# Kernel optimization log

Hardware: AMD Instinct MI355X
Metric: run time of the kernel (lower is better)

The kernel has to match this reference:

```python
import jax, jax.numpy as jnp
import numpy as np

NUM_LEVELS = 4
RADIUS = 4


def _sample1d(vol, x):
    """Linear interpolation along width with zeros padding (grid_sample bilinear,
    align_corners=True, on a height-1 image reduces to this).
    vol: [N, W], x: [N, S] absolute x-coordinates. Returns [N, S]."""
    W = vol.shape[1]
    x0 = jnp.floor(x)
    t = x - x0
    i0 = x0.astype(jnp.int32)
    i1 = i0 + 1

    def gather(i):
        v = jnp.take_along_axis(vol, jnp.clip(i, 0, W - 1), axis=1)
        return jnp.where((i >= 0) & (i < W), v, jnp.zeros_like(v))

    return gather(i0) * (1.0 - t) + gather(i1) * t


def setup_inputs() -> dict:
    key = jax.random.key(0)
    k1, k2, k3 = jax.random.split(key, 3)
    B, C, h, w = 4, 256, 96, 320
    fmap1 = jax.random.normal(k1, (B, C, h, w), dtype=jnp.float32)
    fmap2 = jax.random.normal(k2, (B, C, h, w), dtype=jnp.float32)
    # absolute x-coordinates of centroids, in [0, w-1]
    centroids_coords = jax.random.uniform(k3, (B, 1, h, w), dtype=jnp.float32) * (w - 1)
    return {"fmap1": fmap1, "fmap2": fmap2, "centroids_coords": centroids_coords}


def reference(fmap1, fmap2, centroids_coords):
    B, C, h, w = fmap1.shape
    # 1D correlation volume: dot product over channels, per row, all width pairs
    corr = jnp.einsum('bchw,bchv->bhwv', fmap1, fmap2)  # [B, h, w, w]
    corr = corr / jnp.sqrt(jnp.asarray(C, fmap1.dtype))
    vol = corr.reshape(B * h * w, w)  # [N, w], one 1D row-correlation per query pixel

    cent = centroids_coords.transpose(0, 2, 3, 1).reshape(B * h * w)  # [N]
    side = 2 * RADIUS + 1
    di = jnp.linspace(-RADIUS, RADIUS, side).astype(fmap1.dtype)  # [side]

    outs = []
    for lvl in range(NUM_LEVELS):
        x = cent[:, None] + di[None, :]  # [N, side] absolute coords at this level
        outs.append(_sample1d(vol, x).reshape(B, h, w, side))
        if lvl < NUM_LEVELS - 1:
            Wl = vol.shape[1]
            # avg_pool2d kernel (1,2) stride (1,2) along width
            vol = vol[:, : (Wl // 2) * 2].reshape(vol.shape[0], Wl // 2, 2).mean(axis=2)
            cent = cent / 2.0

    corr_features = jnp.concatenate(outs, axis=-1).transpose(0, 3, 1, 2)
    return corr_features  # [B, num_levels*(2r+1), h, w]
```

## Files before the change

### kernel.cpp

```cpp
#include <hip/hip_runtime.h>

#define W_ 320
#define H_ 96
#define B_ 4
#define C_ 256
#define CS (H_ * W_)
#define MT_ 160
#define PITCH 34
#define PITCHC 321
#define ABUF (MT_ * PITCH)
#define BBUF (W_ * PITCH)
#define TBUF (ABUF + BBUF)

typedef __attribute__((ext_vector_type(8))) short short8;
typedef __attribute__((ext_vector_type(4))) float f32x4;

static __device__ __forceinline__ unsigned f2bf(float f) {
  unsigned u = __builtin_bit_cast(unsigned, f);
  return (u + 0x7FFFu + ((u >> 16) & 1u)) >> 16;
}
static __device__ __forceinline__ unsigned pk(float a, float b) {
  return f2bf(a) | (f2bf(b) << 16);
}
static __device__ __forceinline__ float bf2f(unsigned short h) {
  return __builtin_bit_cast(float, (unsigned)h << 16);
}

union Frag { short8 s; uint4 u; };

__global__ __launch_bounds__(512, 2) void corr_row(
    const float* __restrict__ fmap1, const float* __restrict__ fmap2,
    const float* __restrict__ cents, float* __restrict__ out)
{
  __shared__ __align__(16) unsigned short smem[2 * TBUF];
  unsigned short* Csh = smem;

  const int tid  = threadIdx.x;
  const int lane = tid & 63;
  const int wv   = tid >> 6;
  const int mw   = wv >> 2;
  const int nw   = wv & 3;
  const int m    = lane & 15;
  const int quad = lane >> 4;

  const int i    = blockIdx.x;
  const int r    = ((i >> 4) << 3) | (i & 7);
  const int half = (i >> 3) & 1;
  const int b    = r / H_;
  const int hh   = r % H_;
  const int q0   = half * MT_;

  const float* Abase = fmap1 + ((size_t)b * C_ * H_ + hh) * W_ + q0;
  const float* Bbase = fmap2 + ((size_t)b * C_ * H_ + hh) * W_;

  const float* sp[4];
  int dsti[4];
  int dstsel[4];
  bool act[4];
#pragma unroll
  for (int p = 0; p < 4; ++p) {
    int it = tid + 512 * p;
    act[p] = (it < 1920);
    int c2, v0;
    bool isA = (it < 640);
    if (isA) { c2 = it / 40; v0 = (it % 40) * 4; }
    else     { int ib = it - 640; c2 = ib / 80; v0 = (ib % 80) * 4; }
    if (!act[p]) { c2 = 0; v0 = 0; }
    sp[p]     = (isA ? Abase : Bbase) + (size_t)(2 * c2) * CS + v0;
    dsti[p]   = v0 * 17 + c2;
    dstsel[p] = isA ? 0 : (ABUF / 2);
  }

  f32x4 acc[5][5] = {};
  Frag fa[5];

  float4 g0[4][2], g1[4][2];

  auto issue = [&](int s, float4 (*g)[2]) {
#pragma unroll
    for (int p = 0; p < 4; ++p)
      if (act[p]) {
        const float* q = sp[p] + (size_t)(s * 32) * CS;
        g[p][0] = *(const float4*)q;
        g[p][1] = *(const float4*)(q + CS);
      }
  };
  auto stage = [&](int s, float4 (*g)[2]) {
    unsigned* buf = (unsigned*)(smem + (s & 1) * TBUF);
#pragma unroll
    for (int p = 0; p < 4; ++p)
      if (act[p]) {
        unsigned* d = buf + dstsel[p] + dsti[p];
        d[0]      = pk(g[p][0].x, g[p][1].x);
        d[17]     = pk(g[p][0].y, g[p][1].y);
        d[2 * 17] = pk(g[p][0].z, g[p][1].z);
        d[3 * 17] = pk(g[p][0].w, g[p][1].w);
      }
  };
  auto fragmfma = [&](int s) {
    const unsigned* buf = (const unsigned*)(smem + (s & 1) * TBUF);
#pragma unroll
    for (int mt = 0; mt < 5; ++mt) {
      const unsigned* pa = buf + (mw * 80 + mt * 16 + m) * 17 + quad * 4;
      fa[mt].u.x = pa[0]; fa[mt].u.y = pa[1]; fa[mt].u.z = pa[2]; fa[mt].u.w = pa[3];
    }
#pragma unroll
    for (int nt = 0; nt < 5; ++nt) {
      const unsigned* pb = buf + (ABUF / 2) + (nw * 80 + nt * 16 + m) * 17 + quad * 4;
      Frag fb;
      fb.u.x = pb[0]; fb.u.y = pb[1]; fb.u.z = pb[2]; fb.u.w = pb[3];
#pragma unroll
      for (int mt = 0; mt < 5; ++mt)
        acc[mt][nt] = __builtin_amdgcn_mfma_f32_16x16x32_bf16(
            fa[mt].s, fb.s, acc[mt][nt], 0, 0, 0);
    }
  };

  issue(0, g0);
#pragma unroll
  for (int ss = 0; ss < 4; ++ss) {
    int s = 2 * ss;
    stage(s, g0);
    __syncthreads();
    if (s < 7) issue(s + 1, g1);
    fragmfma(s);

    stage(s + 1, g1);
    __syncthreads();
    if (s + 1 < 7) issue(s + 2, g0);
    fragmfma(s + 1);
  }

#pragma unroll 1
  for (int chunk = 0; chunk < 2; ++chunk) {
    __syncthreads();
    if (mw == chunk) {
#pragma unroll
      for (int mt = 0; mt < 5; ++mt)
#pragma unroll
        for (int nt = 0; nt < 5; ++nt)
#pragma unroll
          for (int rr = 0; rr < 4; ++rr)
            Csh[(mt * 16 + quad * 4 + rr) * PITCHC + nw * 80 + nt * 16 + m] =
                (unsigned short)f2bf(acc[mt][nt][rr] * 0.0625f);
    }
    __syncthreads();
    if (tid < 320) {
      const int l = tid / 80;
      const int q = tid % 80;
      const int qg = q0 + chunk * 80 + q;
      const int Wl  = W_ >> l;
      const int mul = 1 << l;
      const float invm = 1.0f / (float)mul;
      const float cent = cents[(b * H_ + hh) * W_ + qg];
      const float cl = cent * invm;
      const unsigned short* crow = Csh + q * PITCHC;
      float* op = out + ((size_t)(b * 36 + l * 9) * H_ + hh) * W_ + qg;
#pragma unroll
      for (int j = 0; j < 9; ++j) {
        float x  = cl + (float)(j - 4);
        float x0 = floorf(x);
        float t  = x - x0;
        int i0 = (int)x0;
        float v0 = 0.0f, v1 = 0.0f;
        if (i0 >= 0 && i0 < Wl) {
          float s2 = 0.0f;
          for (int d = 0; d < mul; ++d) s2 += bf2f(crow[i0 * mul + d]);
          v0 = s2 * invm;
        }
        int i1 = i0 + 1;
        if (i1 >= 0 && i1 < Wl) {
          float s2 = 0.0f;
          for (int d = 0; d < mul; ++d) s2 += bf2f(crow[i1 * mul + d]);
          v1 = s2 * invm;
        }
        op[(size_t)j * H_ * W_] = v0 * (1.0f - t) + v1 * t;
      }
    }
  }
}

extern "C" void kernel_launch(void* const* d_in, const int* in_sizes, int n_in,
                              void* d_out, int out_size, void* d_ws, size_t ws_size,
                              hipStream_t stream) {
  const float* fmap1 = (const float*)d_in[0];
  const float* fmap2 = (const float*)d_in[1];
  const float* cents = (const float*)d_in[2];
  float* out = (float*)d_out;
  corr_row<<<dim3(768), 512, 0, stream>>>(fmap1, fmap2, cents, out);
}
```

Baseline: 311.9 us.

## Deepen global prefetch, use hardware bf16 pack, and permute LDS layout

Global loads are now issued two stages ahead, with both register buffers in flight, and a custom barrier waits only on LDS counters so outstanding vector memory loads are not drained at each sync. The fp32-to-bf16 packing uses the v_cvt_pk_bf16_f32 instruction instead of manual rounding arithmetic. The LDS staging layout is permuted so that consecutive float4 elements are written with a strided row mapping, aimed at cutting bank conflicts on stores, and the fragment read indices are remapped to match. The risks are that the manual waitcnt/barrier asm may violate compiler ordering assumptions, and that the hardware conversion may round differently.

```diff
diff --git a/kernel.cpp b/kernel.cpp
--- a/kernel.cpp
+++ b/kernel.cpp
@@ -6,6 +6,7 @@
 #define C_ 256
 #define CS (H_ * W_)
 #define MT_ 160
+#define PITCHD 17
 #define PITCH 34
 #define PITCHC 321
 #define ABUF (MT_ * PITCH)
@@ -20,10 +21,15 @@
   return (u + 0x7FFFu + ((u >> 16) & 1u)) >> 16;
 }
 static __device__ __forceinline__ unsigned pk(float a, float b) {
-  return f2bf(a) | (f2bf(b) << 16);
+  unsigned r;
+  asm("v_cvt_pk_bf16_f32 %0, %1, %2" : "=v"(r) : "v"(a), "v"(b));
+  return r;
 }
 static __device__ __forceinline__ float bf2f(unsigned short h) {
   return __builtin_bit_cast(float, (unsigned)h << 16);
+}
+static __device__ __forceinline__ void bar_keepvm() {
+  asm volatile("s_waitcnt lgkmcnt(0)\n\ts_barrier" ::: "memory");
 }
 
 union Frag { short8 s; uint4 u; };
@@ -55,21 +61,20 @@
 
   const float* sp[4];
   int dsti[4];
-  int dstsel[4];
   bool act[4];
 #pragma unroll
   for (int p = 0; p < 4; ++p) {
     int it = tid + 512 * p;
     act[p] = (it < 1920);
-    int c2, v0;
     bool isA = (it < 640);
-    if (isA) { c2 = it / 40; v0 = (it % 40) * 4; }
-    else     { int ib = it - 640; c2 = ib / 80; v0 = (ib % 80) * 4; }
-    if (!act[p]) { c2 = 0; v0 = 0; }
-    sp[p]     = (isA ? Abase : Bbase) + (size_t)(2 * c2) * CS + v0;
-    dsti[p]   = v0 * 17 + c2;
-    dstsel[p] = isA ? 0 : (ABUF / 2);
+    int c2, k;
+    if (isA) { c2 = it / 40; k = it % 40; }
+    else     { int ib = it - 640; c2 = ib / 80; k = ib % 80; }
+    if (!act[p]) { c2 = 0; k = 0; }
+    sp[p]   = (isA ? Abase : Bbase) + (size_t)(2 * c2) * CS + 4 * k;
+    dsti[p] = k * PITCHD + c2 + (isA ? 0 : ABUF / 2);
   }
+  const int st1 = (tid < 128) ? 40 * PITCHD : 80 * PITCHD;
 
   f32x4 acc[5][5] = {};
   Frag fa[5];
@@ -90,23 +95,28 @@
 #pragma unroll
     for (int p = 0; p < 4; ++p)
       if (act[p]) {
-        unsigned* d = buf + dstsel[p] + dsti[p];
+        unsigned* d = buf + dsti[p];
+        const int st = (p == 0) ? 40 * PITCHD : (p >= 2 ? 80 * PITCHD : st1);
         d[0]      = pk(g[p][0].x, g[p][1].x);
-        d[17]     = pk(g[p][0].y, g[p][1].y);
-        d[2 * 17] = pk(g[p][0].z, g[p][1].z);
-        d[3 * 17] = pk(g[p][0].w, g[p][1].w);
+        d[st]     = pk(g[p][0].y, g[p][1].y);
+        d[2 * st] = pk(g[p][0].z, g[p][1].z);
+        d[3 * st] = pk(g[p][0].w, g[p][1].w);
       }
   };
+
+  const int pbA = (m & 3) * 40 + mw * 20 + (m >> 2);
+  const int pbB = (m & 3) * 80 + nw * 20 + (m >> 2);
+
   auto fragmfma = [&](int s) {
     const unsigned* buf = (const unsigned*)(smem + (s & 1) * TBUF);
 #pragma unroll
     for (int mt = 0; mt < 5; ++mt) {
-      const unsigned* pa = buf + (mw * 80 + mt * 16 + m) * 17 + quad * 4;
+      const unsigned* pa = buf + (pbA + mt * 4) * PITCHD + quad * 4;
       fa[mt].u.x = pa[0]; fa[mt].u.y = pa[1]; fa[mt].u.z = pa[2]; fa[mt].u.w = pa[3];
     }
 #pragma unroll
     for (int nt = 0; nt < 5; ++nt) {
-      const unsigned* pb = buf + (ABUF / 2) + (nw * 80 + nt * 16 + m) * 17 + quad * 4;
+      const unsigned* pb = buf + (ABUF / 2) + (pbB + nt * 4) * PITCHD + quad * 4;
       Frag fb;
       fb.u.x = pb[0]; fb.u.y = pb[1]; fb.u.z = pb[2]; fb.u.w = pb[3];
 #pragma unroll
@@ -117,18 +127,19 @@
   };
 
   issue(0, g0);
-#pragma unroll
-  for (int ss = 0; ss < 4; ++ss) {
-    int s = 2 * ss;
-    stage(s, g0);
-    __syncthreads();
-    if (s < 7) issue(s + 1, g1);
-    fragmfma(s);
-
-    stage(s + 1, g1);
-    __syncthreads();
-    if (s + 1 < 7) issue(s + 2, g0);
-    fragmfma(s + 1);
+  issue(1, g1);
+#pragma unroll
+  for (int hs = 0; hs < 8; ++hs) {
+    if (hs & 1) {
+      stage(hs, g1);
+      bar_keepvm();
+      if (hs < 6) issue(hs + 2, g1);
+    } else {
+      stage(hs, g0);
+      bar_keepvm();
+      if (hs < 6) issue(hs + 2, g0);
+    }
+    fragmfma(hs);
   }
 
 #pragma unroll 1
```

Measured after the change: 336.8 us. 1.08x slower.
